# Performance work log

Hardware: AMD Instinct MI355X
Metric: run time of the kernel (lower is better)

The kernel has to match this reference:

```python
import jax, jax.numpy as jnp
import numpy as np
import math

ALPHA, BETA = 0.0, 0.1  # MarketRelation defaults


def setup_inputs() -> dict:
    key = jax.random.key(0)
    ks = jax.random.split(key, 15)
    n, T, d, K, C = 1024, 8, 64, 8, 64
    h = d  # hidden = (2*infeat)//2 = infeat
    s = 0.1
    u = jax.random.uniform(ks[13], (n, n, K), jnp.float32, 1e-6, 1.0 - 1e-6)
    return {
        "x":   jax.random.normal(ks[0], (n, T, d), jnp.float32),
        "Ind": jax.random.uniform(ks[1], (n, n), jnp.float32),
        "Loc": jax.random.uniform(ks[2], (n, n), jnp.float32),
        "a":   jax.random.normal(ks[3], (T, 1), jnp.float32),
        "W1m": jax.random.normal(ks[4], (2 * d, h), jnp.float32) * s,
        "b1m": jax.random.normal(ks[5], (h,), jnp.float32) * s,
        "W2m": jax.random.normal(ks[6], (h, 1), jnp.float32) * s,
        "b2m": jax.random.normal(ks[7], (1,), jnp.float32) * s,
        "W1s": jax.random.normal(ks[8], (2 * d, h), jnp.float32) * s,
        "b1s": jax.random.normal(ks[9], (h,), jnp.float32) * s,
        "W2s": jax.random.normal(ks[10], (h, K), jnp.float32) * s,
        "b2s": jax.random.normal(ks[11], (K,), jnp.float32) * s,
        "E":   jax.random.normal(ks[12], (K, n, C), jnp.float32) * s,
        "g":   -jnp.log(-jnp.log(u)),  # Gumbel(0,1) noise for gumbel_softmax
    }


def reference(x, Ind, Loc, a, W1m, b1m, W2m, b2m, W1s, b1s, W2s, b2s, E, g):
    n, T, d = x.shape
    # --- MarketRelation ---
    # fc1(concat(x_j, x_k)) == x_j @ W1m[:d] + x_k @ W1m[d:] + b1m (same math,
    # avoids materializing the N x N x 2d concat tensor)
    W1a, W1b = W1m[:d], W1m[d:]
    a_soft = jax.nn.softmax(a, axis=0)  # [T,1]
    A_mkt = jnp.zeros((n, n), x.dtype)
    for i in range(T):
        xi = x[:, i, :]                      # [n,d]
        hA = xi @ W1a                        # [n,h]
        hB = xi @ W1b                        # [n,h]
        hmat = jax.nn.relu(hA[:, None, :] + hB[None, :, :] + b1m)  # [n,n,h]
        adj = jax.nn.relu(hmat @ W2m + b2m)[..., 0]                # [n,n]
        factor = 1.0 + ALPHA * math.exp(-BETA * (T - i - 1))
        A_mkt = A_mkt + adj * (a_soft[i, 0] * factor)
    # --- NobsRelation (on last timestep) ---
    xl = x[:, -1, :]
    Ws1a, Ws1b = W1s[:d], W1s[d:]
    hs = jax.nn.relu((xl @ Ws1a)[:, None, :] + (xl @ Ws1b)[None, :, :] + b1s)
    logits = jax.nn.relu(hs @ W2s + b2s)          # [n,n,K]
    y = jax.nn.softmax(logits + g, axis=-1)       # gumbel_softmax, tau=1, soft
    D = jnp.einsum('knc,kmc->nmk', E, E)          # stack of E_k E_k^T, [n,n,K]
    A_nobs = jnp.sum(D * y, axis=-1)              # [n,n]
    return jnp.stack([Ind, Loc, A_mkt, A_nobs])   # [4,n,n]
```

## Files before the change

kernel.cpp:

```cpp
#include <hip/hip_runtime.h>

typedef unsigned short USH;
typedef float v2f __attribute__((ext_vector_type(2)));

__device__ __forceinline__ float bf2f(USH u) {
    return __uint_as_float(((unsigned int)u) << 16);
}
__device__ __forceinline__ float lo16(unsigned int u) { return __uint_as_float(u << 16); }
__device__ __forceinline__ float hi16(unsigned int u) { return __uint_as_float(u & 0xFFFF0000u); }
__device__ __forceinline__ USH f2bf(float f) {
    unsigned int i = __float_as_uint(f);
    i += 0x7FFFu + ((i >> 16) & 1u);
    return (USH)(i >> 16);
}
__device__ __forceinline__ v2f relu2(v2f s) {
    return __builtin_elementwise_max(s, (v2f)(0.0f));
}

__device__ __forceinline__ float ldf(const void* p, long idx, int bf) {
    return bf ? bf2f(((const USH*)p)[idx]) : ((const float*)p)[idx];
}
__device__ __forceinline__ void ld4(const void* p, long idx, int bf, float o[4]) {
    if (bf) {
        ushort4 u = *(const ushort4*)((const USH*)p + idx);
        o[0] = bf2f(u.x); o[1] = bf2f(u.y); o[2] = bf2f(u.z); o[3] = bf2f(u.w);
    } else {
        float4 v = *(const float4*)((const float*)p + idx);
        o[0] = v.x; o[1] = v.y; o[2] = v.z; o[3] = v.w;
    }
}

__device__ __forceinline__ int detect_bf(const void* ind) {
    const uint4* p = (const uint4*)ind;
    unsigned o = 0;
    #pragma unroll
    for (int i = 0; i < 8; ++i) { uint4 v = p[i]; o |= v.x | v.y | v.z | v.w; }
    return (o & 0x8000u) == 0;
}

__global__ __launch_bounds__(256) void k_pre_d(
    const void* __restrict__ x,
    const void* __restrict__ W1m,
    const void* __restrict__ b1m,
    const void* __restrict__ W1s,
    const void* __restrict__ b1s,
    const void* __restrict__ E,
    const void* __restrict__ IndDet,
    USH* __restrict__ hA, USH* __restrict__ hBb,
    USH* __restrict__ hsA, USH* __restrict__ hsBb,
    USH* __restrict__ D)
{
    __shared__ float smem[8192];
    float* sA = smem;
    float* sB = smem + 4096;
    const int bf = detect_bf(IndDet);
    const int tid = threadIdx.x;
    const int bid = blockIdx.x;
    const int tx = tid & 15, ty = tid >> 4;

    if (bid < 2048) {
        const int mb = (bid & 15) * 64, nb = ((bid >> 4) & 15) * 64, k = bid >> 8;
        const long ek = (long)k * 65536;
        {
            const int r_l = tid >> 2, cq = tid & 3;
            const long bn = ek + (long)(nb + r_l) * 64 + cq * 16;
            const long bm = ek + (long)(mb + r_l) * 64 + cq * 16;
            #pragma unroll
            for (int j = 0; j < 4; ++j) {
                const int c0 = cq * 16 + j * 4;
                float o[4];
                ld4(E, bn + j * 4, bf, o);
                #pragma unroll
                for (int e = 0; e < 4; ++e) sA[(c0 + e) * 64 + r_l] = o[e];
                ld4(E, bm + j * 4, bf, o);
                #pragma unroll
                for (int e = 0; e < 4; ++e) sB[(c0 + e) * 64 + r_l] = o[e];
            }
        }
        __syncthreads();
        const int m0 = tx * 4, n0 = ty * 4;
        float acc[4][4] = {};
        #pragma unroll 8
        for (int c = 0; c < 64; ++c) {
            const float4 an = *(const float4*)&sA[c * 64 + n0];
            const float4 am = *(const float4*)&sB[c * 64 + m0];
            const float aa[4] = {an.x, an.y, an.z, an.w};
            const float bb[4] = {am.x, am.y, am.z, am.w};
            #pragma unroll
            for (int ni = 0; ni < 4; ++ni)
                #pragma unroll
                for (int mi = 0; mi < 4; ++mi)
                    acc[ni][mi] += aa[ni] * bb[mi];
        }
        #pragma unroll
        for (int ni = 0; ni < 4; ++ni) {
            ushort4 o;
            o.x = f2bf(acc[ni][0]); o.y = f2bf(acc[ni][1]);
            o.z = f2bf(acc[ni][2]); o.w = f2bf(acc[ni][3]);
            *(ushort4*)&D[(long)k * 1048576 + (long)(nb + n0 + ni) * 1024 + mb + m0] = o;
        }
    } else {
        const int bid2 = bid - 2048;
        const int nbase = (bid2 & 15) * 64;
        const int by = bid2 >> 4;
        int t, rb;
        const void* Wsrc;
        const void* bias;
        USH* dst;
        if (by < 8)        { t = by;     rb = 0;  Wsrc = W1m; bias = nullptr; dst = hA + by * 65536; }
        else if (by < 16)  { t = by - 8; rb = 64; Wsrc = W1m; bias = b1m;     dst = hBb + (by - 8) * 65536; }
        else if (by == 16) { t = 7;      rb = 0;  Wsrc = W1s; bias = nullptr; dst = hsA; }
        else               { t = 7;      rb = 64; Wsrc = W1s; bias = b1s;     dst = hsBb; }

        {
            const int n_l = tid >> 2, dq = tid & 3;
            const long base = (long)(nbase + n_l) * 512 + t * 64 + dq * 16;
            #pragma unroll
            for (int j = 0; j < 4; ++j) {
                float o[4]; ld4(x, base + j * 4, bf, o);
                const int d0 = dq * 16 + j * 4;
                #pragma unroll
                for (int e = 0; e < 4; ++e) sA[(d0 + e) * 64 + n_l] = o[e];
            }
        }
        {
            const int d_l = tid >> 2, cq = tid & 3;
            const long base = (long)(rb + d_l) * 64 + cq * 16;
            #pragma unroll
            for (int j = 0; j < 4; ++j) {
                float o[4]; ld4(Wsrc, base + j * 4, bf, o);
                const int c0 = cq * 16 + j * 4;
                #pragma unroll
                for (int e = 0; e < 4; ++e) sB[d_l * 64 + c0 + e] = o[e];
            }
        }
        __syncthreads();

        const int c0 = tx * 4, nq = ty * 4;
        float acc[4][4] = {};
        #pragma unroll 16
        for (int d = 0; d < 64; ++d) {
            const float4 xa = *(const float4*)&sA[d * 64 + nq];
            const float4 wv = *(const float4*)&sB[d * 64 + c0];
            const float aa[4] = {xa.x, xa.y, xa.z, xa.w};
            const float ww[4] = {wv.x, wv.y, wv.z, wv.w};
            #pragma unroll
            for (int ci = 0; ci < 4; ++ci)
                #pragma unroll
                for (int ni = 0; ni < 4; ++ni)
                    acc[ci][ni] += ww[ci] * aa[ni];
        }
        #pragma unroll
        for (int ci = 0; ci < 4; ++ci) {
            const float bb = bias ? ldf(bias, c0 + ci, bf) : 0.0f;
            ushort4 o;
            o.x = f2bf(acc[ci][0] + bb); o.y = f2bf(acc[ci][1] + bb);
            o.z = f2bf(acc[ci][2] + bb); o.w = f2bf(acc[ci][3] + bb);
            *(ushort4*)&dst[(c0 + ci) * 1024 + nbase + nq] = o;
        }
    }
}

__global__ __launch_bounds__(512, 4) void k_main(
    const USH* __restrict__ hA, const USH* __restrict__ hBb,
    const USH* __restrict__ hsA, const USH* __restrict__ hsBb,
    const USH* __restrict__ Dm,
    const void* __restrict__ Ind, const void* __restrict__ Loc,
    const void* __restrict__ a, const void* __restrict__ W2m,
    const void* __restrict__ b2m, const void* __restrict__ W2s,
    const void* __restrict__ b2s, const void* __restrict__ g,
    void* __restrict__ out)
{
    __shared__ USH As[2][64 * 64];
    __shared__ USH Bs[2][64 * 32];
    __shared__ float w2s_l[64 * 8];
    __shared__ float w2m_l[64];
    __shared__ float asoft_l[8];

    const int bf = detect_bf(Ind);
    const int tid = threadIdx.x;
    const int mb = blockIdx.x * 32, nb = blockIdx.y * 64;
    const int tx = tid & 15, ty = tid >> 4;
    const int m0 = tx * 2, n0 = ty * 2;

    if (tid < 64) w2m_l[tid] = ldf(W2m, tid, bf);
    if (tid >= 64 && tid < 192) {
        const int q = tid - 64;
        float o[4]; ld4(W2s, q * 4, bf, o);
        #pragma unroll
        for (int e = 0; e < 4; ++e) w2s_l[q * 4 + e] = o[e];
    }
    if (tid < 8) {
        float av[8], mx = -1e30f, s = 0.0f;
        #pragma unroll
        for (int k = 0; k < 8; ++k) { av[k] = ldf(a, k, bf); mx = fmaxf(mx, av[k]); }
        #pragma unroll
        for (int k = 0; k < 8; ++k) s += __expf(av[k] - mx);
        asoft_l[tid] = __expf(av[tid] - mx) / s;
    }
    const float b2m_f = ldf(b2m, 0, bf);

    const int offA = (tid >> 3) * 1024 + nb + (tid & 7) * 8;
    const int offB = (tid >> 3) * 1024 + mb + (tid & 7) * 4;
    const int ldsA = tid * 8, ldsB = tid * 4;

    {
        uint4 pa = *(const uint4*)(hA + offA);
        uint2 pb = *(const uint2*)(hBb + offB);
        *(uint4*)&As[0][ldsA] = pa;
        *(uint2*)&Bs[0][ldsB] = pb;
    }
    __syncthreads();

    v2f amk2[2] = {(v2f)(0.0f), (v2f)(0.0f)};

    for (int t = 0; t < 8; ++t) {
        const int cur = t & 1, nxt = cur ^ 1;
        const USH* srcA = (t < 7) ? (hA + (t + 1) * 65536) : hsA;
        const USH* srcB = (t < 7) ? (hBb + (t + 1) * 65536) : hsBb;
        const uint4 pa = *(const uint4*)(srcA + offA);
        const uint2 pb = *(const uint2*)(srcB + offB);

        v2f acc2[2] = {(v2f)(0.0f), (v2f)(0.0f)};
        #pragma unroll 8
        for (int c = 0; c < 64; ++c) {
            const unsigned uA = *(const unsigned*)&As[cur][(c << 6) + n0];
            const unsigned uB = *(const unsigned*)&Bs[cur][(c << 5) + m0];
            v2f bb; bb.x = lo16(uB); bb.y = hi16(uB);
            const float w = w2m_l[c];
            const v2f wv = (v2f)(w);
            const v2f s0 = relu2((v2f)(lo16(uA)) + bb);
            const v2f s1 = relu2((v2f)(hi16(uA)) + bb);
            acc2[0] = __builtin_elementwise_fma(s0, wv, acc2[0]);
            acc2[1] = __builtin_elementwise_fma(s1, wv, acc2[1]);
        }
        const v2f asv = (v2f)(asoft_l[t]);
        const v2f b2v = (v2f)(b2m_f);
        amk2[0] = __builtin_elementwise_fma(relu2(acc2[0] + b2v), asv, amk2[0]);
        amk2[1] = __builtin_elementwise_fma(relu2(acc2[1] + b2v), asv, amk2[1]);

        *(uint4*)&As[nxt][ldsA] = pa;
        *(uint2*)&Bs[nxt][ldsB] = pb;
        __syncthreads();
    }

    v2f lgp[2][8];
    #pragma unroll
    for (int i = 0; i < 2; ++i)
        #pragma unroll
        for (int k = 0; k < 8; ++k) lgp[i][k] = (v2f)(0.0f);

    #pragma unroll 4
    for (int c = 0; c < 64; ++c) {
        const unsigned uA = *(const unsigned*)&As[0][(c << 6) + n0];
        const unsigned uB = *(const unsigned*)&Bs[0][(c << 5) + m0];
        v2f bb; bb.x = lo16(uB); bb.y = hi16(uB);
        const v2f z0 = relu2((v2f)(lo16(uA)) + bb);
        const v2f z1 = relu2((v2f)(hi16(uA)) + bb);
        const float4 wa = *(const float4*)&w2s_l[c << 3];
        const float4 wb = *(const float4*)&w2s_l[(c << 3) + 4];
        const float wk[8] = {wa.x, wa.y, wa.z, wa.w, wb.x, wb.y, wb.z, wb.w};
        #pragma unroll
        for (int k = 0; k < 8; ++k) {
            const v2f wkv = (v2f)(wk[k]);
            lgp[0][k] = __builtin_elementwise_fma(z0, wkv, lgp[0][k]);
            lgp[1][k] = __builtin_elementwise_fma(z1, wkv, lgp[1][k]);
        }
    }

    float b2s_f[8];
    #pragma unroll
    for (int k = 0; k < 8; ++k) b2s_f[k] = ldf(b2s, k, bf);

    #pragma unroll
    for (int i = 0; i < 2; ++i) {
        const long rowoff = (long)(nb + n0 + i) * 1024 + mb + m0;
        float gv[16];
        ld4(g, rowoff * 8 + 0, bf, gv + 0);
        ld4(g, rowoff * 8 + 4, bf, gv + 4);
        ld4(g, rowoff * 8 + 8, bf, gv + 8);
        ld4(g, rowoff * 8 + 12, bf, gv + 12);

        float s0 = 0.0f, s1 = 0.0f, d0 = 0.0f, d1 = 0.0f;
        #pragma unroll
        for (int k = 0; k < 8; ++k) {
            const v2f lr = relu2(lgp[i][k] + (v2f)(b2s_f[k]));
            const float e0 = __expf(lr.x + gv[k]);
            const float e1 = __expf(lr.y + gv[8 + k]);
            s0 += e0; s1 += e1;
            const ushort2 dv = *(const ushort2*)&Dm[((long)k << 20) + rowoff];
            d0 += bf2f(dv.x) * e0;
            d1 += bf2f(dv.y) * e1;
        }

        if (bf) {
            USH* o = (USH*)out;
            *(ushort2*)&o[rowoff] = *(const ushort2*)&((const USH*)Ind)[rowoff];
            *(ushort2*)&o[1048576 + rowoff] = *(const ushort2*)&((const USH*)Loc)[rowoff];
            ushort2 o2; o2.x = f2bf(amk2[i].x); o2.y = f2bf(amk2[i].y);
            *(ushort2*)&o[2 * 1048576 + rowoff] = o2;
            ushort2 o3; o3.x = f2bf(d0 / s0); o3.y = f2bf(d1 / s1);
            *(ushort2*)&o[3 * 1048576 + rowoff] = o3;
        } else {
            float* o = (float*)out;
            *(float2*)&o[rowoff] = *(const float2*)&((const float*)Ind)[rowoff];
            *(float2*)&o[1048576 + rowoff] = *(const float2*)&((const float*)Loc)[rowoff];
            float2 o2; o2.x = amk2[i].x; o2.y = amk2[i].y;
            *(float2*)&o[2 * 1048576 + rowoff] = o2;
            float2 o3; o3.x = d0 / s0; o3.y = d1 / s1;
            *(float2*)&o[3 * 1048576 + rowoff] = o3;
        }
    }
}

extern "C" void kernel_launch(void* const* d_in, const int* in_sizes, int n_in,
                              void* d_out, int out_size, void* d_ws, size_t ws_size,
                              hipStream_t stream) {
    const void* x   = d_in[0];
    const void* Ind = d_in[1];
    const void* Loc = d_in[2];
    const void* a   = d_in[3];
    const void* W1m = d_in[4];
    const void* b1m = d_in[5];
    const void* W2m = d_in[6];
    const void* b2m = d_in[7];
    const void* W1s = d_in[8];
    const void* b1s = d_in[9];
    const void* W2s = d_in[10];
    const void* b2s = d_in[11];
    const void* E   = d_in[12];
    const void* g   = d_in[13];

    USH* ws   = (USH*)d_ws;
    USH* hA   = ws;
    USH* hBb  = hA + 524288;
    USH* hsA  = hBb + 524288;
    USH* hsBb = hsA + 65536;
    USH* Dm   = hsBb + 65536;

    k_pre_d<<<dim3(2336), 256, 0, stream>>>(x, W1m, b1m, W1s, b1s, E, Ind,
                                            hA, hBb, hsA, hsBb, Dm);
    k_main<<<dim3(32, 16), 512, 0, stream>>>(hA, hBb, hsA, hsBb, Dm,
                                             Ind, Loc, a, W2m, b2m, W2s, b2s,
                                             g, d_out);
}
```

Measured before the change: 194.8 us.

## Store hidden tiles as fp32 in LDS and use 32x32 blocks of 256 threads

The main kernel now widens the bf16 hidden-activation tiles to fp32 once, when they are written to shared memory, so the inner loops no longer unpack bf16 values on every read. The output tile drops from 64x32 to 32x32 with 256 threads per block, which doubles the grid to 1024 blocks. W2m weights are read as float4 groups and the inner loop is fully unrolled. In exchange, the LDS footprint per element doubles and each block handles a smaller tile, so more global loads of hA and hB are repeated across blocks.

New measurement: 187.1 us. 3.9% less time.

```diff
diff --git a/kernel.cpp b/kernel.cpp
--- a/kernel.cpp
+++ b/kernel.cpp
@@ -161,7 +161,7 @@
     }
 }
 
-__global__ __launch_bounds__(512, 4) void k_main(
+__global__ __launch_bounds__(256, 4) void k_main(
     const USH* __restrict__ hA, const USH* __restrict__ hBb,
     const USH* __restrict__ hsA, const USH* __restrict__ hsBb,
     const USH* __restrict__ Dm,
@@ -171,15 +171,15 @@
     const void* __restrict__ b2s, const void* __restrict__ g,
     void* __restrict__ out)
 {
-    __shared__ USH As[2][64 * 64];
-    __shared__ USH Bs[2][64 * 32];
+    __shared__ float As[2][64 * 32];
+    __shared__ float Bs[2][64 * 32];
     __shared__ float w2s_l[64 * 8];
     __shared__ float w2m_l[64];
     __shared__ float asoft_l[8];
 
     const int bf = detect_bf(Ind);
     const int tid = threadIdx.x;
-    const int mb = blockIdx.x * 32, nb = blockIdx.y * 64;
+    const int mb = blockIdx.x * 32, nb = blockIdx.y * 32;
     const int tx = tid & 15, ty = tid >> 4;
     const int m0 = tx * 2, n0 = ty * 2;
 
@@ -200,15 +200,20 @@
     }
     const float b2m_f = ldf(b2m, 0, bf);
 
-    const int offA = (tid >> 3) * 1024 + nb + (tid & 7) * 8;
-    const int offB = (tid >> 3) * 1024 + mb + (tid & 7) * 4;
-    const int ldsA = tid * 8, ldsB = tid * 4;
+    const int offA = (tid >> 2) * 1024 + nb + (tid & 3) * 8;
+    const int offB = (tid >> 2) * 1024 + mb + (tid & 3) * 8;
+    const int ldsOff = tid * 8;
 
     {
-        uint4 pa = *(const uint4*)(hA + offA);
-        uint2 pb = *(const uint2*)(hBb + offB);
-        *(uint4*)&As[0][ldsA] = pa;
-        *(uint2*)&Bs[0][ldsB] = pb;
+        const uint4 pa = *(const uint4*)(hA + offA);
+        const uint4 pb = *(const uint4*)(hBb + offB);
+        float4 fa0, fa1, fb0, fb1;
+        fa0.x = lo16(pa.x); fa0.y = hi16(pa.x); fa0.z = lo16(pa.y); fa0.w = hi16(pa.y);
+        fa1.x = lo16(pa.z); fa1.y = hi16(pa.z); fa1.z = lo16(pa.w); fa1.w = hi16(pa.w);
+        fb0.x = lo16(pb.x); fb0.y = hi16(pb.x); fb0.z = lo16(pb.y); fb0.w = hi16(pb.y);
+        fb1.x = lo16(pb.z); fb1.y = hi16(pb.z); fb1.z = lo16(pb.w); fb1.w = hi16(pb.w);
+        *(float4*)&As[0][ldsOff] = fa0; *(float4*)&As[0][ldsOff + 4] = fa1;
+        *(float4*)&Bs[0][ldsOff] = fb0; *(float4*)&Bs[0][ldsOff + 4] = fb1;
     }
     __syncthreads();
 
@@ -219,28 +224,37 @@
         const USH* srcA = (t < 7) ? (hA + (t + 1) * 65536) : hsA;
         const USH* srcB = (t < 7) ? (hBb + (t + 1) * 65536) : hsBb;
         const uint4 pa = *(const uint4*)(srcA + offA);
-        const uint2 pb = *(const uint2*)(srcB + offB);
+        const uint4 pb = *(const uint4*)(srcB + offB);
 
         v2f acc2[2] = {(v2f)(0.0f), (v2f)(0.0f)};
-        #pragma unroll 8
-        for (int c = 0; c < 64; ++c) {
-            const unsigned uA = *(const unsigned*)&As[cur][(c << 6) + n0];
-            const unsigned uB = *(const unsigned*)&Bs[cur][(c << 5) + m0];
-            v2f bb; bb.x = lo16(uB); bb.y = hi16(uB);
-            const float w = w2m_l[c];
-            const v2f wv = (v2f)(w);
-            const v2f s0 = relu2((v2f)(lo16(uA)) + bb);
-            const v2f s1 = relu2((v2f)(hi16(uA)) + bb);
-            acc2[0] = __builtin_elementwise_fma(s0, wv, acc2[0]);
-            acc2[1] = __builtin_elementwise_fma(s1, wv, acc2[1]);
+        #pragma unroll
+        for (int c4 = 0; c4 < 16; ++c4) {
+            const float4 wq = *(const float4*)&w2m_l[c4 * 4];
+            const float ww[4] = {wq.x, wq.y, wq.z, wq.w};
+            #pragma unroll
+            for (int j = 0; j < 4; ++j) {
+                const int c = c4 * 4 + j;
+                const v2f aa = *(const v2f*)&As[cur][(c << 5) + n0];
+                const v2f bb = *(const v2f*)&Bs[cur][(c << 5) + m0];
+                const v2f wv = (v2f)(ww[j]);
+                const v2f s0 = relu2((v2f)(aa.x) + bb);
+                const v2f s1 = relu2((v2f)(aa.y) + bb);
+                acc2[0] = __builtin_elementwise_fma(s0, wv, acc2[0]);
+                acc2[1] = __builtin_elementwise_fma(s1, wv, acc2[1]);
+            }
         }
         const v2f asv = (v2f)(asoft_l[t]);
         const v2f b2v = (v2f)(b2m_f);
         amk2[0] = __builtin_elementwise_fma(relu2(acc2[0] + b2v), asv, amk2[0]);
         amk2[1] = __builtin_elementwise_fma(relu2(acc2[1] + b2v), asv, amk2[1]);
 
-        *(uint4*)&As[nxt][ldsA] = pa;
-        *(uint2*)&Bs[nxt][ldsB] = pb;
+        float4 f0, f1;
+        f0.x = lo16(pa.x); f0.y = hi16(pa.x); f0.z = lo16(pa.y); f0.w = hi16(pa.y);
+        f1.x = lo16(pa.z); f1.y = hi16(pa.z); f1.z = lo16(pa.w); f1.w = hi16(pa.w);
+        *(float4*)&As[nxt][ldsOff] = f0; *(float4*)&As[nxt][ldsOff + 4] = f1;
+        f0.x = lo16(pb.x); f0.y = hi16(pb.x); f0.z = lo16(pb.y); f0.w = hi16(pb.y);
+        f1.x = lo16(pb.z); f1.y = hi16(pb.z); f1.z = lo16(pb.w); f1.w = hi16(pb.w);
+        *(float4*)&Bs[nxt][ldsOff] = f0; *(float4*)&Bs[nxt][ldsOff + 4] = f1;
         __syncthreads();
     }
 
@@ -252,11 +266,10 @@
 
     #pragma unroll 4
     for (int c = 0; c < 64; ++c) {
-        const unsigned uA = *(const unsigned*)&As[0][(c << 6) + n0];
-        const unsigned uB = *(const unsigned*)&Bs[0][(c << 5) + m0];
-        v2f bb; bb.x = lo16(uB); bb.y = hi16(uB);
-        const v2f z0 = relu2((v2f)(lo16(uA)) + bb);
-        const v2f z1 = relu2((v2f)(hi16(uA)) + bb);
+        const v2f aa = *(const v2f*)&As[0][(c << 5) + n0];
+        const v2f bb = *(const v2f*)&Bs[0][(c << 5) + m0];
+        const v2f z0 = relu2((v2f)(aa.x) + bb);
+        const v2f z1 = relu2((v2f)(aa.y) + bb);
         const float4 wa = *(const float4*)&w2s_l[c << 3];
         const float4 wb = *(const float4*)&w2s_l[(c << 3) + 4];
         const float wk[8] = {wa.x, wa.y, wa.z, wa.w, wb.x, wb.y, wb.z, wb.w};
@@ -340,7 +353,7 @@
 
     k_pre_d<<<dim3(2336), 256, 0, stream>>>(x, W1m, b1m, W1s, b1s, E, Ind,
                                             hA, hBb, hsA, hsBb, Dm);
-    k_main<<<dim3(32, 16), 512, 0, stream>>>(hA, hBb, hsA, hsBb, Dm,
+    k_main<<<dim3(32, 32), 256, 0, stream>>>(hA, hBb, hsA, hsBb, Dm,
                                              Ind, Loc, a, W2m, b2m, W2s, b2s,
                                              g, d_out);
 }
```
